# Performance work log

Hardware: AMD Instinct MI355X
Metric: run time of the kernel (lower is better)

Reference implementation:

```python
import jax, jax.numpy as jnp
import numpy as np

N = 100000        # nodes
E_RAND = 1500000  # random edges (self loops appended -> E = 1.6M)
IN_DIM = 500
HID = 256
NCLASS = 50
K = 10


def setup_inputs() -> dict:
    key = jax.random.key(0)
    ks = jax.random.split(key, 8)
    feats = jax.random.normal(ks[0], (N, IN_DIM), dtype=jnp.float32)
    # edges: random + self loops (fit() adds self loops)
    src_r = jax.random.randint(ks[1], (E_RAND,), 0, N, dtype=jnp.int32)
    dst_r = jax.random.randint(ks[2], (E_RAND,), 0, N, dtype=jnp.int32)
    loop = jnp.arange(N, dtype=jnp.int32)
    src = jnp.concatenate([src_r, loop])
    dst = jnp.concatenate([dst_r, loop])
    # params (xavier-uniform-like scales)
    def xavier(k, shape):
        lim = np.sqrt(6.0 / (shape[0] + shape[1]))
        return jax.random.uniform(k, shape, jnp.float32, -lim, lim)
    W1 = xavier(ks[3], (IN_DIM, HID))
    b1 = jnp.zeros((HID,), jnp.float32)
    W2 = xavier(ks[4], (HID, NCLASS))
    b2 = jnp.zeros((NCLASS,), jnp.float32)
    s = xavier(ks[5], (NCLASS, 1))
    return {"feats": feats, "W1": W1, "b1": b1, "W2": W2, "b2": b2,
            "s": s, "src": src, "dst": dst}


def reference(feats, W1, b1, W2, b2, s, src, dst):
    # --- MLP (dropout is identity in eval / p=0) ---
    x = jax.nn.relu(feats @ W1 + b1)          # [N, HID]
    x = x @ W2 + b2                            # [N, NCLASS]
    # --- DAGNNConv: k-hop sym-normalized propagation ---
    deg = jax.ops.segment_sum(jnp.ones_like(dst, dtype=jnp.float32), dst,
                              num_segments=N)  # in-degrees
    norm = jnp.power(deg, -0.5)[:, None]       # [N, 1]
    results = [x]
    h = x
    for _ in range(K):
        h = h * norm
        h = jax.ops.segment_sum(h[src], dst, num_segments=N)  # copy_u + sum
        h = h * norm
        results.append(h)
    H = jnp.stack(results, axis=1)             # [N, K+1, C]
    S = jax.nn.sigmoid(jnp.einsum('nkc,co->nk', H, s))  # [N, K+1]
    out = jnp.einsum('nk,nkc->nc', S, H)       # [N, C]
    return out
```

## Files before the change

kernel.cpp:

```cpp
#include <hip/hip_runtime.h>
#include <hip/hip_bf16.h>
#include <math.h>

#define NN     100000
#define INDIM  500
#define HID    256
#define NCLASS 50
#define KHOPS  10
#define KPAD   512
#define CPAD   64

static inline size_t roundup256(size_t x) { return (x + 255) & ~(size_t)255; }

typedef __attribute__((ext_vector_type(8))) short bf16x8;
typedef __attribute__((ext_vector_type(4))) float f32x4;
typedef __attribute__((ext_vector_type(4))) short short4v;

typedef __attribute__((address_space(3))) unsigned       lds_u32;
typedef const __attribute__((address_space(1))) unsigned glb_u32;

__device__ inline short f2bf(float f) {
    union { float f; unsigned u; } v; v.f = f;
    unsigned r = v.u + 0x7FFFu + ((v.u >> 16) & 1u);
    return (short)(r >> 16);
}
__device__ inline short f2bf_hw(float f) {
    __hip_bfloat16 h = __float2bfloat16(f);
    return *reinterpret_cast<short*>(&h);
}
__device__ inline float bflo(unsigned u) {
    union { unsigned u; float f; } v; v.u = u << 16; return v.f;
}
__device__ inline float bfhi(unsigned u) {
    union { unsigned u; float f; } v; v.u = u & 0xFFFF0000u; return v.f;
}
__device__ inline unsigned packbf(float a, float b) {
    return (unsigned)(unsigned short)f2bf(a) | ((unsigned)(unsigned short)f2bf(b) << 16);
}

__global__ void dagnn_zero2(int* __restrict__ a, int* __restrict__ b, int n) {
    int i = blockIdx.x * blockDim.x + threadIdx.x;
    if (i < n) { a[i] = 0; b[i] = 0; }
}

__global__ void dagnn_deg(const int* __restrict__ dst, int* __restrict__ degi, int E) {
    int e = blockIdx.x * blockDim.x + threadIdx.x;
    if (e < E) atomicAdd(&degi[dst[e]], 1);
}

__global__ void dagnn_norm(const int* __restrict__ degi, float* __restrict__ nrm, int n) {
    int i = blockIdx.x * blockDim.x + threadIdx.x;
    if (i < n) nrm[i] = rsqrtf((float)degi[i]);
}

__global__ void dagnn_scan(const int* __restrict__ degi, int* __restrict__ rowptr, int n) {
    __shared__ int wsum[16];
    __shared__ int carry_s;
    const int tid  = threadIdx.x;
    const int lane = tid & 63;
    const int wid  = tid >> 6;
    if (tid == 0) carry_s = 0;
    __syncthreads();
    for (int base = 0; base < n; base += 4096) {
        int i0 = base + tid * 4;
        int v0 = (i0 + 0 < n) ? degi[i0 + 0] : 0;
        int v1 = (i0 + 1 < n) ? degi[i0 + 1] : 0;
        int v2 = (i0 + 2 < n) ? degi[i0 + 2] : 0;
        int v3 = (i0 + 3 < n) ? degi[i0 + 3] : 0;
        int tsum = v0 + v1 + v2 + v3;
        int x = tsum;
        #pragma unroll
        for (int off = 1; off < 64; off <<= 1) {
            int t = __shfl_up(x, off);
            if (lane >= off) x += t;
        }
        if (lane == 63) wsum[wid] = x;
        __syncthreads();
        if (tid == 0) {
            int run = carry_s;
            #pragma unroll
            for (int w = 0; w < 16; ++w) { int t = wsum[w]; wsum[w] = run; run += t; }
            carry_s = run;
        }
        __syncthreads();
        int texcl = wsum[wid] + (x - tsum);
        if (i0 + 0 < n) rowptr[i0 + 0] = texcl;
        if (i0 + 1 < n) rowptr[i0 + 1] = texcl + v0;
        if (i0 + 2 < n) rowptr[i0 + 2] = texcl + v0 + v1;
        if (i0 + 3 < n) rowptr[i0 + 3] = texcl + v0 + v1 + v2;
        __syncthreads();
    }
    if (tid == 0) rowptr[n] = carry_s;
}

__global__ void dagnn_fill(const int* __restrict__ src, const int* __restrict__ dst,
                           const int* __restrict__ rowptr, int* __restrict__ fillc,
                           int* __restrict__ colidx, int E) {
    int e = blockIdx.x * blockDim.x + threadIdx.x;
    if (e >= E) return;
    int d = dst[e];
    int pos = rowptr[d] + atomicAdd(&fillc[d], 1);
    colidx[pos] = src[e];
}

__global__ void dagnn_w1ts(const float* __restrict__ W1, short* __restrict__ Bts) {
    int idx = blockIdx.x * 256 + threadIdx.x;
    if (idx >= HID * KPAD) return;
    int ks = idx >> 13;
    int n  = (idx >> 5) & 255;
    int kk = idx & 31;
    int k  = ks * 32 + kk;
    float v = (k < INDIM) ? W1[(size_t)k * HID + n] : 0.f;
    Bts[idx] = f2bf(v);
}

__global__ void dagnn_w2t(const float* __restrict__ W2, short* __restrict__ W2t) {
    int idx = blockIdx.x * 256 + threadIdx.x;
    if (idx >= CPAD * HID) return;
    int n = idx >> 8;
    int k = idx & 255;
    float v = (n < NCLASS) ? W2[(size_t)k * NCLASS + n] : 0.f;
    W2t[idx] = f2bf(v);
}

__global__ void dagnn_sgate(const float* __restrict__ svec, float2* __restrict__ sg) {
    int c = threadIdx.x;
    if (c < 32) {
        float x = (2 * c     < NCLASS) ? svec[2 * c]     : 0.f;
        float y = (2 * c + 1 < NCLASS) ? svec[2 * c + 1] : 0.f;
        sg[c] = make_float2(x, y);
    }
}

#define G1_STAGE(ABASE, BBASE, KS)                                             \
    {                                                                          \
        const int k0_ = (KS) * 32;                                             \
        _Pragma("unroll")                                                      \
        for (int j = 0; j < 2; ++j) {                                          \
            int slot = (wid * 2 + j) * 64 + lane;                              \
            int mrow = slot >> 3;                                  \
            int q    = (slot & 7) ^ (mrow & 7);    \
            int gm   = row0 + mrow;                                            \
            int gk   = k0_ + q * 4;                                            \
            const float* asrc = (gm < M && gk < INDIM)                         \
                ? (A + (size_t)gm * INDIM + gk) : A;                           \
            __builtin_amdgcn_global_load_lds((glb_u32*)asrc,                   \
                (lds_u32*)((ABASE) + (wid * 2 + j) * 256), 16, 0, 0);          \
            const short* bsrc = Bts + ((size_t)(KS) << 13) + slot * 8;         \
            __builtin_amdgcn_global_load_lds((glb_u32*)bsrc,                   \
                (lds_u32*)((BBASE) + (wid * 2 + j) * 512), 16, 0, 0);          \
        }                                                                      \
    }

__global__ __launch_bounds__(512, 4) void dagnn_gemm1_mfma(
        const float* __restrict__ A, const short* __restrict__ Bts,
        const float* __restrict__ bias, short* __restrict__ C, int M) {
    __shared__ __align__(16) char smem[67584];
    float* As0 = (float*)smem;
    float* As1 = (float*)(smem + 16384);
    short* Bs0 = (short*)(smem + 32768);
    short* Bs1 = (short*)(smem + 49152);
    short* Ep  = (short*)smem;

    const int tid  = threadIdx.x;
    const int lane = tid & 63;
    const int wid  = tid >> 6;
    const int l16  = lane & 15;
    const int quad = lane >> 4;
    const int m_off = (wid & 1) * 64;
    const int n_off = (wid >> 1) * 64;
    const int row0  = blockIdx.x * 128;

    f32x4 acc[4][4] = {};

    G1_STAGE(As0, Bs0, 0)
    __syncthreads();

    for (int ks = 0; ks < KPAD / 32; ++ks) {
        const int cur = ks & 1;
        const float* ab = cur ? As1 : As0;
        const short* bb = cur ? Bs1 : Bs0;
        if (ks + 1 < KPAD / 32) {
            if (cur) { G1_STAGE(As0, Bs0, ks + 1) }
            else     { G1_STAGE(As1, Bs1, ks + 1) }
        }

        bf16x8 bfr[4];
        #pragma unroll
        for (int nt = 0; nt < 4; ++nt)
            bfr[nt] = *(const bf16x8*)(bb + (n_off + nt * 16 + l16) * 32 + quad * 8);

        #pragma unroll
        for (int mt = 0; mt < 4; ++mt) {
            int m  = m_off + mt * 16 + l16;
            int s0 = (quad * 2 + 0) ^ (m & 7);
            int s1 = (quad * 2 + 1) ^ (m & 7);
            float4 lo = *(const float4*)(ab + m * 32 + s0 * 4);
            float4 hi = *(const float4*)(ab + m * 32 + s1 * 4);
            bf16x8 af;
            af[0] = f2bf_hw(lo.x); af[1] = f2bf_hw(lo.y);
            af[2] = f2bf_hw(lo.z); af[3] = f2bf_hw(lo.w);
            af[4] = f2bf_hw(hi.x); af[5] = f2bf_hw(hi.y);
            af[6] = f2bf_hw(hi.z); af[7] = f2bf_hw(hi.w);
            #pragma unroll
            for (int nt = 0; nt < 4; ++nt)
                acc[mt][nt] = __builtin_amdgcn_mfma_f32_16x16x32_bf16(
                                  af, bfr[nt], acc[mt][nt], 0, 0, 0);
        }
        __syncthreads();
    }

    float bv[4];
    #pragma unroll
    for (int nt = 0; nt < 4; ++nt) bv[nt] = bias[n_off + nt * 16 + l16];

    #pragma unroll
    for (int mt = 0; mt < 4; ++mt) {
        #pragma unroll
        for (int nt = 0; nt < 4; ++nt) {
            #pragma unroll
            for (int r = 0; r < 4; ++r) {
                float v = acc[mt][nt][r] + bv[nt];
                v = v > 0.f ? v : 0.f;
                float vp = __shfl_xor(v, 1);
                if (!(l16 & 1)) {
                    int mrel = m_off + mt * 16 + quad * 4 + r;
                    *(unsigned*)(Ep + mrel * 264 + n_off + nt * 16 + l16) =
                        packbf(v, vp);
                }
            }
        }
    }
    __syncthreads();
    #pragma unroll
    for (int it = 0; it < 8; ++it) {
        int cidx = tid + it * 512;
        int rr   = cidx >> 5;
        int chk  = cidx & 31;
        int gm   = row0 + rr;
        if (gm < M)
            *(bf16x8*)(C + (size_t)gm * HID + chk * 8) =
                *(const bf16x8*)(Ep + rr * 264 + chk * 8);
    }
}

#define A2_STRIDE 72
#define B2_STRIDE 264
__global__ __launch_bounds__(256) void dagnn_mlp2_mfma(
        const short* __restrict__ hid, const short* __restrict__ W2t,
        const float* __restrict__ b2, const float* __restrict__ svec,
        const float* __restrict__ nrm,
        unsigned* __restrict__ hs0, float* __restrict__ out, int M) {
    __shared__ __align__(16) short As[128 * A2_STRIDE];
    __shared__ __align__(16) short Bs[CPAD * B2_STRIDE];

    const int tid  = threadIdx.x;
    const int lane = tid & 63;
    const int wid  = tid >> 6;
    const int l16  = lane & 15;
    const int quad = lane >> 4;
    const int m_off = wid * 32;
    const int row0  = blockIdx.x * 128;

    #pragma unroll
    for (int it = 0; it < 8; ++it) {
        int slot = tid + it * 256;
        int n   = slot >> 5;
        int seg = slot & 31;
        bf16x8 b = *(const bf16x8*)(W2t + (size_t)n * HID + seg * 8);
        *(bf16x8*)&Bs[n * B2_STRIDE + seg * 8] = b;
    }

    f32x4 acc[2][4] = {};

    for (int ks = 0; ks < HID / 64; ++ks) {
        const int k0 = ks * 64;
        #pragma unroll
        for (int it = 0; it < 4; ++it) {
            int slot = tid + it * 256;
            int m   = slot >> 3;
            int seg = slot & 7;
            int gm  = row0 + m;
            bf16x8 v = {};
            if (gm < M) v = *(const bf16x8*)(hid + (size_t)gm * HID + k0 + seg * 8);
            *(bf16x8*)&As[m * A2_STRIDE + seg * 8] = v;
        }
        __syncthreads();

        #pragma unroll
        for (int ksub = 0; ksub < 2; ++ksub) {
            bf16x8 af[2], bfr[4];
            #pragma unroll
            for (int mt = 0; mt < 2; ++mt)
                af[mt] = *(const bf16x8*)&As[(m_off + mt * 16 + l16) * A2_STRIDE
                                             + ksub * 32 + quad * 8];
            #pragma unroll
            for (int nt = 0; nt < 4; ++nt)
                bfr[nt] = *(const bf16x8*)&Bs[(nt * 16 + l16) * B2_STRIDE
                                              + k0 + ksub * 32 + quad * 8];
            #pragma unroll
            for (int mt = 0; mt < 2; ++mt)
                #pragma unroll
                for (int nt = 0; nt < 4; ++nt)
                    acc[mt][nt] = __builtin_amdgcn_mfma_f32_16x16x32_bf16(
                                      af[mt], bfr[nt], acc[mt][nt], 0, 0, 0);
        }
        __syncthreads();
    }

    float b2v[4], ssv[4];
    #pragma unroll
    for (int nt = 0; nt < 4; ++nt) {
        int gc = nt * 16 + l16;
        b2v[nt] = (gc < NCLASS) ? b2[gc]   : 0.f;
        ssv[nt] = (gc < NCLASS) ? svec[gc] : 0.f;
    }
    #pragma unroll
    for (int mt = 0; mt < 2; ++mt) {
        #pragma unroll
        for (int r = 0; r < 4; ++r) {
            int gm = row0 + m_off + mt * 16 + quad * 4 + r;
            float xv[4], q = 0.f;
            #pragma unroll
            for (int nt = 0; nt < 4; ++nt) {
                xv[nt] = acc[mt][nt][r] + b2v[nt];
                q += xv[nt] * ssv[nt];
            }
            #pragma unroll
            for (int off = 1; off < 16; off <<= 1) q += __shfl_xor(q, off);
            float S = 1.f / (1.f + __expf(-q));
            float nd = (gm < M) ? nrm[gm] : 0.f;
            #pragma unroll
            for (int nt = 0; nt < 4; ++nt) {
                int gc = nt * 16 + l16;
                float hv = xv[nt] * nd;
                float hp = __shfl_xor(hv, 1);
                if (gm < M) {
                    if (!(l16 & 1))
                        hs0[(size_t)gm * 32 + nt * 8 + (l16 >> 1)] = packbf(hv, hp);
                    if (gc < NCLASS) out[(size_t)gm * NCLASS + gc] = S * xv[nt];
                }
            }
        }
    }
}

__global__ __launch_bounds__(256) void dagnn_prop7(
        const unsigned* __restrict__ hs, const float* __restrict__ nrm,
        const int* __restrict__ rowptr, const int* __restrict__ colidx,
        const float2* __restrict__ sgate, unsigned* __restrict__ hs_next,
        float* __restrict__ out, int M, int write_next) {
    const int lane = threadIdx.x & 63;
    const int wid  = threadIdx.x >> 6;
    const int d    = blockIdx.x * 4 + wid;
    if (d >= M) return;
    const int half = lane >> 5;
    const int c    = lane & 31;
    const int beg = rowptr[d], end = rowptr[d + 1];
    const float nd = nrm[d];

    const int ch = 2 * c;
    float o0 = 0.f, o1 = 0.f;
    if (half == 0 && ch < NCLASS) {
        o0 = out[(size_t)d * NCLASS + ch];
        o1 = out[(size_t)d * NCLASS + ch + 1];
    }

    float a0 = 0.f, a1 = 0.f;
    int e = beg;
    for (; e + 16 <= end; e += 16) {
        int s[8];
        #pragma unroll
        for (int t = 0; t < 8; ++t)
            s[t] = __builtin_nontemporal_load(&colidx[e + half + 2 * t]);
        unsigned u[8];
        #pragma unroll
        for (int t = 0; t < 8; ++t)
            u[t] = hs[(size_t)s[t] * 32 + c];
        #pragma unroll
        for (int t = 0; t < 8; ++t) { a0 += bflo(u[t]); a1 += bfhi(u[t]); }
    }
    if (e < end) {
        int s[8];
        #pragma unroll
        for (int t = 0; t < 8; ++t) {
            int ei = e + half + 2 * t;
            s[t] = (ei < end) ? __builtin_nontemporal_load(&colidx[ei]) : -1;
        }
        #pragma unroll
        for (int t = 0; t < 8; ++t) {
            if (s[t] >= 0) {
                unsigned u = hs[(size_t)s[t] * 32 + c];
                a0 += bflo(u); a1 += bfhi(u);
            }
        }
    }

    a0 += __shfl_xor(a0, 32);
    a1 += __shfl_xor(a1, 32);

    float r0 = a0 * nd, r1 = a1 * nd;
    float2 g = sgate[c];
    float p = r0 * g.x + r1 * g.y;
    #pragma unroll
    for (int off = 16; off; off >>= 1) p += __shfl_xor(p, off);
    float S = 1.f / (1.f + __expf(-p));
    if (half == 0) {
        if (write_next) hs_next[(size_t)d * 32 + c] = packbf(r0 * nd, r1 * nd);
        if (ch < NCLASS) {
            out[(size_t)d * NCLASS + ch]     = o0 + S * r0;
            out[(size_t)d * NCLASS + ch + 1] = o1 + S * r1;
        }
    }
}

extern "C" void kernel_launch(void* const* d_in, const int* in_sizes, int n_in,
                              void* d_out, int out_size, void* d_ws, size_t ws_size,
                              hipStream_t stream) {
    const float* feats = (const float*)d_in[0];
    const float* W1    = (const float*)d_in[1];
    const float* b1    = (const float*)d_in[2];
    const float* W2    = (const float*)d_in[3];
    const float* b2    = (const float*)d_in[4];
    const float* svec  = (const float*)d_in[5];
    const int*   src   = (const int*)d_in[6];
    const int*   dst   = (const int*)d_in[7];
    float* out = (float*)d_out;

    const int M = in_sizes[0] / INDIM;
    const int E = in_sizes[6];

    char* p = (char*)d_ws;
    size_t off = 0;
    short*    hid   = (short*)   (p + off); off += roundup256((size_t)M * HID * 2);
    unsigned* hsA   = (unsigned*)(p + off); off += roundup256((size_t)M * 32 * 4);
    unsigned* hsB   = (unsigned*)(p + off); off += roundup256((size_t)M * 32 * 4);
    short*    W1t   = (short*)   (p + off); off += roundup256((size_t)HID * KPAD * 2);
    short*    W2t   = (short*)   (p + off); off += roundup256((size_t)CPAD * HID * 2);
    float2*   sgate = (float2*)  (p + off); off += roundup256(32 * sizeof(float2));
    int*      degi  = (int*)     (p + off); off += roundup256((size_t)M * 4);
    float*    nrm   = (float*)   (p + off); off += roundup256((size_t)M * 4);
    int*      rowptr= (int*)     (p + off); off += roundup256((size_t)(M + 1) * 4);
    int*      fillc = (int*)     (p + off); off += roundup256((size_t)M * 4);
    int*      colidx= (int*)     (p + off); off += roundup256((size_t)E * 4);
    (void)ws_size;

    dagnn_zero2<<<(M + 255) / 256, 256, 0, stream>>>(degi, fillc, M);
    dagnn_deg<<<(E + 255) / 256, 256, 0, stream>>>(dst, degi, E);
    dagnn_norm<<<(M + 255) / 256, 256, 0, stream>>>(degi, nrm, M);
    dagnn_scan<<<1, 1024, 0, stream>>>(degi, rowptr, M);
    dagnn_fill<<<(E + 255) / 256, 256, 0, stream>>>(src, dst, rowptr, fillc, colidx, E);

    dagnn_w1ts<<<(HID * KPAD + 255) / 256, 256, 0, stream>>>(W1, W1t);
    dagnn_w2t<<<(CPAD * HID + 255) / 256, 256, 0, stream>>>(W2, W2t);
    dagnn_sgate<<<1, 32, 0, stream>>>(svec, sgate);

    dagnn_gemm1_mfma<<<(M + 127) / 128, 512, 0, stream>>>(feats, W1t, b1, hid, M);
    dagnn_mlp2_mfma<<<(M + 127) / 128, 256, 0, stream>>>(hid, W2t, b2, svec, nrm,
                                                         hsA, out, M);

    unsigned* hin = hsA;
    unsigned* hout = hsB;
    for (int k = 0; k < KHOPS; ++k) {
        dagnn_prop7<<<(M + 3) / 4, 256, 0, stream>>>(hin, nrm, rowptr, colidx,
                                                     sgate, hout, out, M,
                                                     k < KHOPS - 1);
        unsigned* t = hin; hin = hout; hout = t;
    }
}
```

Before: 1.167 ms.

## Fuse all propagation hops into one persistent kernel with a grid barrier

Replaces ten per-hop propagation launches with a single persistent kernel. Each half-wave owns nine destination rows across all hops, ping-pongs between the two hidden buffers, and uses a sense-reversing atomic grid barrier between hops. The gated output sum stays in registers and is written to `out` once at the end, rather than read and written every hop. This removes launch gaps and repeated output traffic. In exchange, rows are processed serially within each half-wave, there is less latency hiding per gather, and correctness relies on all blocks being co-resident; the bounded spin escape would break ordering if they are not.

```diff
diff --git a/kernel.cpp b/kernel.cpp
--- a/kernel.cpp
+++ b/kernel.cpp
@@ -345,71 +345,104 @@
     }
 }
 
-__global__ __launch_bounds__(256) void dagnn_prop7(
-        const unsigned* __restrict__ hs, const float* __restrict__ nrm,
-        const int* __restrict__ rowptr, const int* __restrict__ colidx,
-        const float2* __restrict__ sgate, unsigned* __restrict__ hs_next,
-        float* __restrict__ out, int M, int write_next) {
+__device__ __forceinline__ void dagnn_gridbar(int* cnt, int* sense, int nblk) {
+    __syncthreads();
+    if (threadIdx.x == 0) {
+        int my = __hip_atomic_load(sense, __ATOMIC_RELAXED, __HIP_MEMORY_SCOPE_AGENT);
+        int a  = __hip_atomic_fetch_add(cnt, 1, __ATOMIC_ACQ_REL, __HIP_MEMORY_SCOPE_AGENT);
+        if (a == nblk - 1) {
+            __hip_atomic_store(cnt, 0, __ATOMIC_RELAXED, __HIP_MEMORY_SCOPE_AGENT);
+            __hip_atomic_store(sense, my ^ 1, __ATOMIC_RELEASE, __HIP_MEMORY_SCOPE_AGENT);
+        } else {
+            long spin = 0;
+            while (__hip_atomic_load(sense, __ATOMIC_RELAXED,
+                                     __HIP_MEMORY_SCOPE_AGENT) == my) {
+                __builtin_amdgcn_s_sleep(2);
+                if (++spin > (1L << 30)) break;
+            }
+            __threadfence();
+        }
+    }
+    __syncthreads();
+}
+
+#define PROPF_RPH 9
+__global__ __launch_bounds__(256, 6) void dagnn_propf(
+        unsigned* __restrict__ hsA, unsigned* __restrict__ hsB,
+        const float* __restrict__ nrm, const int* __restrict__ rowptr,
+        const int* __restrict__ colidx, const float2* __restrict__ sgate,
+        float* __restrict__ out, int M, int nblk,
+        int* __restrict__ bcnt, int* __restrict__ bsense) {
     const int lane = threadIdx.x & 63;
     const int wid  = threadIdx.x >> 6;
-    const int d    = blockIdx.x * 4 + wid;
-    if (d >= M) return;
     const int half = lane >> 5;
     const int c    = lane & 31;
-    const int beg = rowptr[d], end = rowptr[d + 1];
-    const float nd = nrm[d];
+    const int halfId = (blockIdx.x * 4 + wid) * 2 + half;
+    const int d0 = halfId * PROPF_RPH;
+    const float2 g = sgate[c];
+
+    float oa0[PROPF_RPH], oa1[PROPF_RPH];
+    #pragma unroll
+    for (int r = 0; r < PROPF_RPH; ++r) { oa0[r] = 0.f; oa1[r] = 0.f; }
+
+    for (int hop = 0; hop < KHOPS; ++hop) {
+        const unsigned* hin  = (hop & 1) ? hsB : hsA;
+        unsigned*       hout = (hop & 1) ? hsA : hsB;
+        #pragma unroll
+        for (int r = 0; r < PROPF_RPH; ++r) {
+            const int d = d0 + r;
+            if (d < M) {
+                const int beg = rowptr[d], end = rowptr[d + 1];
+                const float nd = nrm[d];
+                float a0 = 0.f, a1 = 0.f;
+                int sc[8];
+                #pragma unroll
+                for (int t = 0; t < 8; ++t) {
+                    int ei = beg + t;
+                    sc[t] = (ei < end) ? colidx[ei] : -1;
+                }
+                for (int e = beg;;) {
+                    const int en = e + 8;
+                    const bool more = en < end;
+                    int sn[8];
+                    #pragma unroll
+                    for (int t = 0; t < 8; ++t) {
+                        int ei = en + t;
+                        sn[t] = (more && ei < end) ? colidx[ei] : -1;
+                    }
+                    #pragma unroll
+                    for (int t = 0; t < 8; ++t) {
+                        if (sc[t] >= 0) {
+                            unsigned u = hin[(size_t)sc[t] * 32 + c];
+                            a0 += bflo(u); a1 += bfhi(u);
+                        }
+                    }
+                    if (!more) break;
+                    #pragma unroll
+                    for (int t = 0; t < 8; ++t) sc[t] = sn[t];
+                    e = en;
+                }
+                const float r0 = a0 * nd, r1 = a1 * nd;
+                float p = r0 * g.x + r1 * g.y;
+                #pragma unroll
+                for (int off = 1; off < 32; off <<= 1) p += __shfl_xor(p, off);
+                const float S = 1.f / (1.f + __expf(-p));
+                if (hop < KHOPS - 1)
+                    hout[(size_t)d * 32 + c] = packbf(r0 * nd, r1 * nd);
+                oa0[r] += S * r0;
+                oa1[r] += S * r1;
+            }
+        }
+        if (hop < KHOPS - 1) dagnn_gridbar(bcnt, bsense, nblk);
+    }
 
     const int ch = 2 * c;
-    float o0 = 0.f, o1 = 0.f;
-    if (half == 0 && ch < NCLASS) {
-        o0 = out[(size_t)d * NCLASS + ch];
-        o1 = out[(size_t)d * NCLASS + ch + 1];
-    }
-
-    float a0 = 0.f, a1 = 0.f;
-    int e = beg;
-    for (; e + 16 <= end; e += 16) {
-        int s[8];
-        #pragma unroll
-        for (int t = 0; t < 8; ++t)
-            s[t] = __builtin_nontemporal_load(&colidx[e + half + 2 * t]);
-        unsigned u[8];
-        #pragma unroll
-        for (int t = 0; t < 8; ++t)
-            u[t] = hs[(size_t)s[t] * 32 + c];
-        #pragma unroll
-        for (int t = 0; t < 8; ++t) { a0 += bflo(u[t]); a1 += bfhi(u[t]); }
-    }
-    if (e < end) {
-        int s[8];
-        #pragma unroll
-        for (int t = 0; t < 8; ++t) {
-            int ei = e + half + 2 * t;
-            s[t] = (ei < end) ? __builtin_nontemporal_load(&colidx[ei]) : -1;
-        }
-        #pragma unroll
-        for (int t = 0; t < 8; ++t) {
-            if (s[t] >= 0) {
-                unsigned u = hs[(size_t)s[t] * 32 + c];
-                a0 += bflo(u); a1 += bfhi(u);
-            }
-        }
-    }
-
-    a0 += __shfl_xor(a0, 32);
-    a1 += __shfl_xor(a1, 32);
-
-    float r0 = a0 * nd, r1 = a1 * nd;
-    float2 g = sgate[c];
-    float p = r0 * g.x + r1 * g.y;
-    #pragma unroll
-    for (int off = 16; off; off >>= 1) p += __shfl_xor(p, off);
-    float S = 1.f / (1.f + __expf(-p));
-    if (half == 0) {
-        if (write_next) hs_next[(size_t)d * 32 + c] = packbf(r0 * nd, r1 * nd);
-        if (ch < NCLASS) {
-            out[(size_t)d * NCLASS + ch]     = o0 + S * r0;
-            out[(size_t)d * NCLASS + ch + 1] = o1 + S * r1;
+    #pragma unroll
+    for (int r = 0; r < PROPF_RPH; ++r) {
+        const int d = d0 + r;
+        if (d < M && ch < NCLASS) {
+            out[(size_t)d * NCLASS + ch]     += oa0[r];
+            out[(size_t)d * NCLASS + ch + 1] += oa1[r];
         }
     }
 }
@@ -443,9 +476,11 @@
     int*      rowptr= (int*)     (p + off); off += roundup256((size_t)(M + 1) * 4);
     int*      fillc = (int*)     (p + off); off += roundup256((size_t)M * 4);
     int*      colidx= (int*)     (p + off); off += roundup256((size_t)E * 4);
+    int*      bar   = (int*)     (p + off); off += roundup256(2 * sizeof(int));
     (void)ws_size;
 
     dagnn_zero2<<<(M + 255) / 256, 256, 0, stream>>>(degi, fillc, M);
+    dagnn_zero2<<<1, 64, 0, stream>>>(bar, bar + 1, 1);
     dagnn_deg<<<(E + 255) / 256, 256, 0, stream>>>(dst, degi, E);
     dagnn_norm<<<(M + 255) / 256, 256, 0, stream>>>(degi, nrm, M);
     dagnn_scan<<<1, 1024, 0, stream>>>(degi, rowptr, M);
@@ -459,12 +494,7 @@
     dagnn_mlp2_mfma<<<(M + 127) / 128, 256, 0, stream>>>(hid, W2t, b2, svec, nrm,
                                                          hsA, out, M);
 
-    unsigned* hin = hsA;
-    unsigned* hout = hsB;
-    for (int k = 0; k < KHOPS; ++k) {
-        dagnn_prop7<<<(M + 3) / 4, 256, 0, stream>>>(hin, nrm, rowptr, colidx,
-                                                     sgate, hout, out, M,
-                                                     k < KHOPS - 1);
-        unsigned* t = hin; hin = hout; hout = t;
-    }
-}
+    const int nblk = (M + 8 * PROPF_RPH - 1) / (8 * PROPF_RPH);
+    dagnn_propf<<<nblk, 256, 0, stream>>>(hsA, hsB, nrm, rowptr, colidx, sgate,
+                                          out, M, nblk, bar, bar + 1);
+}
```

After: 3.091 ms. 2.65x slower.
